# Optimization experiments

Measured on AMD Instinct MI355X. Metric: run time of the kernel, lower is better.

Reference implementation:

```python
import jax, jax.numpy as jnp
import numpy as np

N_EMBD = 2048
N_HEAD = 16
HEAD_SIZE = N_EMBD // N_HEAD


def setup_inputs() -> dict:
    key = jax.random.key(0)
    k1, k2, k3 = jax.random.split(key, 3)
    x = jax.random.normal(k1, (4, 2048, N_EMBD), dtype=jnp.float32)
    # Linear weights stored as (in, out) for x @ W
    scale = 1.0 / np.sqrt(N_EMBD)
    w_qkv = jax.random.normal(k2, (N_EMBD, 3 * N_EMBD), dtype=jnp.float32) * scale
    w_proj = jax.random.normal(k3, (N_EMBD, N_EMBD), dtype=jnp.float32) * scale
    return {"x": x, "w_qkv": w_qkv, "w_proj": w_proj}


def reference(x, w_qkv, w_proj):
    B, T, C = x.shape
    qkv = x @ w_qkv  # [B, T, 3C]
    q, k, v = jnp.split(qkv, 3, axis=-1)
    # [B, H, T, Dh]
    def heads(t):
        return t.reshape(B, T, N_HEAD, HEAD_SIZE).transpose(0, 2, 1, 3)
    q, k, v = heads(q), heads(k), heads(v)
    scores = jnp.einsum('bhqd,bhkd->bhqk', q, k) * (1.0 / np.sqrt(HEAD_SIZE))
    causal = jnp.tril(jnp.ones((T, T), dtype=bool))
    scores = jnp.where(causal, scores, jnp.finfo(scores.dtype).min)
    att = jax.nn.softmax(scores, axis=-1)
    y = jnp.einsum('bhqk,bhkd->bhqd', att, v)
    y = y.transpose(0, 2, 1, 3).reshape(B, T, C)
    return y @ w_proj
```

## Files before the change

### kernel.cpp

```cpp
#include <hip/hip_runtime.h>

typedef unsigned short u16;
typedef unsigned int u32;
typedef __bf16 bf16x8 __attribute__((ext_vector_type(8)));
typedef float f32x4 __attribute__((ext_vector_type(4)));
typedef u32 u32x4 __attribute__((ext_vector_type(4)));

__device__ __forceinline__ u16 f2bf(float f) {
  u32 u = __builtin_bit_cast(u32, f);
  return (u16)((u + 0x7fffu + ((u >> 16) & 1u)) >> 16);
}

__device__ __forceinline__ f32x4 mfma16(bf16x8 a, bf16x8 b, f32x4 c) {
  return __builtin_amdgcn_mfma_f32_16x16x32_bf16(a, b, c, 0, 0, 0);
}

__device__ __forceinline__ u32 cvtpk_bf16(float lo, float hi) {
  u32 r;
  asm("v_cvt_pk_bf16_f32 %0, %1, %2" : "=v"(r) : "v"(lo), "v"(hi));
  return r;
}

__device__ __forceinline__ float fexp2(float x) {
  float r;
  asm("v_exp_f32 %0, %1" : "=v"(r) : "v"(x));
  return r;
}

struct alignas(8) U16x4 { u16 x, y, z, w; };

#define AS1 __attribute__((address_space(1)))
#define AS3 __attribute__((address_space(3)))
__device__ __forceinline__ void gl16(const u16* g, u16* l) {
  __builtin_amdgcn_global_load_lds((const AS1 u32*)g, (AS3 u32*)l, 16, 0, 0);
}

__global__ __launch_bounds__(256) void k_f32_to_bf16(const float* __restrict__ in,
                                                     u16* __restrict__ out, long n4) {
  long i = (long)blockIdx.x * blockDim.x + threadIdx.x;
  long stride = (long)gridDim.x * blockDim.x;
  for (; i < n4; i += stride) {
    float4 v = ((const float4*)in)[i];
    U16x4 o{f2bf(v.x), f2bf(v.y), f2bf(v.z), f2bf(v.w)};
    ((U16x4*)out)[i] = o;
  }
}

__global__ __launch_bounds__(256) void k_transpose_f32_to_bf16(const float* __restrict__ in,
                                                               u16* __restrict__ out,
                                                               int rows, int cols) {
  __shared__ float tile[64][65];
  int bc = blockIdx.x * 64, br = blockIdx.y * 64;
  int tx = threadIdx.x & 15;
  int ty = threadIdx.x >> 4;
#pragma unroll
  for (int i = 0; i < 4; ++i) {
    int r = ty + i * 16;
    float4 v = *(const float4*)&in[(long)(br + r) * cols + bc + tx * 4];
    tile[r][tx * 4 + 0] = v.x;
    tile[r][tx * 4 + 1] = v.y;
    tile[r][tx * 4 + 2] = v.z;
    tile[r][tx * 4 + 3] = v.w;
  }
  __syncthreads();
#pragma unroll
  for (int i = 0; i < 4; ++i) {
    int c = ty + i * 16;
    int r4 = tx * 4;
    U16x4 o{f2bf(tile[r4 + 0][c]), f2bf(tile[r4 + 1][c]),
            f2bf(tile[r4 + 2][c]), f2bf(tile[r4 + 3][c])};
    *(U16x4*)&out[(long)(bc + c) * rows + br + r4] = o;
  }
}

template <typename OutT, bool WRITE_VT>
__global__ __launch_bounds__(512, 2) void k_gemm256(const u16* __restrict__ A,
                                                    const u16* __restrict__ Bt,
                                                    OutT* __restrict__ C,
                                                    u16* __restrict__ vt,
                                                    int M, int N, int K) {
  __shared__ alignas(16) u16 As[4][8192];
  __shared__ alignas(16) u16 Bs[4][8192];

  int gx = gridDim.x;
  int nwg = gx * gridDim.y;
  int bid = blockIdx.y * gx + blockIdx.x;
  int swz = (bid & 7) * (nwg >> 3) + (bid >> 3);
  int rem = swz % (gx * 4);
  int bx = rem >> 2;
  int by = (swz / (gx * 4)) * 4 + (rem & 3);

  int tid = threadIdx.x;
  int lane = tid & 63;
  int w = tid >> 6;
  int wr = w >> 2, wc = w & 3;
  int lr = lane & 15, lg = lane >> 4;
  long brow = (long)by * 256, bcol = (long)bx * 256;

  int rS[2], cS[2];
#pragma unroll
  for (int i = 0; i < 2; ++i) {
    int q = i * 512 + tid;
    rS[i] = q >> 2;
    cS[i] = ((q & 3) ^ ((rS[i] >> 1) & 3)) << 3;
  }
  const u16* Ab = A + brow * K;
  const u16* Bb = Bt + bcol * K;

  int offA[8], offB[4];
#pragma unroll
  for (int m = 0; m < 8; ++m) {
    int row = wr * 128 + m * 16 + lr;
    offA[m] = row * 32 + ((lg ^ ((row >> 1) & 3)) << 3);
  }
#pragma unroll
  for (int n = 0; n < 4; ++n) {
    int row = wc * 64 + n * 16 + lr;
    offB[n] = row * 32 + ((lg ^ ((row >> 1) & 3)) << 3);
  }

  f32x4 zero = {0.f, 0.f, 0.f, 0.f};
  f32x4 acc[8][4];
#pragma unroll
  for (int m = 0; m < 8; ++m)
#pragma unroll
    for (int n = 0; n < 4; ++n) acc[m][n] = zero;

  int NS = K >> 5;

#define STAGE256(SBUF, KT)                                                          \
  do {                                                                              \
    int kk_ = (KT) << 5;                                                            \
    gl16(Ab + (long)rS[0] * K + kk_ + cS[0], &As[SBUF][(0 * 512 + w * 64) * 8]);    \
    gl16(Ab + (long)rS[1] * K + kk_ + cS[1], &As[SBUF][(1 * 512 + w * 64) * 8]);    \
    gl16(Bb + (long)rS[0] * K + kk_ + cS[0], &Bs[SBUF][(0 * 512 + w * 64) * 8]);    \
    gl16(Bb + (long)rS[1] * K + kk_ + cS[1], &Bs[SBUF][(1 * 512 + w * 64) * 8]);    \
  } while (0)

  STAGE256(0, 0);
  STAGE256(1, 1);
  STAGE256(2, 2);
  asm volatile("s_waitcnt vmcnt(8)" ::: "memory");
  __builtin_amdgcn_s_barrier();

  for (int s = 0; s < NS; ++s) {
    int cb = s & 3;
    bf16x8 af[8], bfn[4];
#pragma unroll
    for (int m = 0; m < 8; ++m) af[m] = *(const bf16x8*)&As[cb][offA[m]];
#pragma unroll
    for (int n = 0; n < 4; ++n) bfn[n] = *(const bf16x8*)&Bs[cb][offB[n]];
    int t = s + 3;
    int tb = t & 3;
    if (t > NS - 1) t = NS - 1;
    STAGE256(tb, t);
    __builtin_amdgcn_s_setprio(1);
#pragma unroll
    for (int m = 0; m < 4; ++m)
#pragma unroll
      for (int n = 0; n < 4; ++n) acc[m][n] = mfma16(af[m], bfn[n], acc[m][n]);
    __builtin_amdgcn_s_setprio(0);
    __builtin_amdgcn_s_setprio(1);
#pragma unroll
    for (int m = 4; m < 8; ++m)
#pragma unroll
      for (int n = 0; n < 4; ++n) acc[m][n] = mfma16(af[m], bfn[n], acc[m][n]);
    __builtin_amdgcn_s_setprio(0);
    asm volatile("s_waitcnt vmcnt(8)" ::: "memory");
    __builtin_amdgcn_s_barrier();
  }
#undef STAGE256
  asm volatile("s_waitcnt vmcnt(0)" ::: "memory");

  if constexpr (WRITE_VT) {
    if (bcol >= 4096) {
      int b_ = (int)(brow >> 11);
      int tb_ = (int)(brow & 2047) + wr * 128;
#pragma unroll
      for (int m = 0; m < 8; ++m)
#pragma unroll
        for (int n = 0; n < 4; ++n) {
          int hd = (int)(bcol - 4096) + wc * 64 + n * 16 + lr;
          int h_ = hd >> 7, d_ = hd & 127;
          U16x4 pk{f2bf(acc[m][n][0]), f2bf(acc[m][n][1]),
                   f2bf(acc[m][n][2]), f2bf(acc[m][n][3])};
          *(U16x4*)(vt + ((long)(b_ * 16 + h_) * 128 + d_) * 2048 + tb_ + m * 16 + lg * 4) = pk;
        }
      return;
    }
  }
#pragma unroll
  for (int m = 0; m < 8; ++m)
#pragma unroll
    for (int n = 0; n < 4; ++n)
#pragma unroll
      for (int r = 0; r < 4; ++r) {
        long row = brow + wr * 128 + m * 16 + lg * 4 + r;
        long col = bcol + wc * 64 + n * 16 + lr;
        float v = acc[m][n][r];
        if constexpr (sizeof(OutT) == 2)
          C[row * N + col] = (OutT)f2bf(v);
        else
          C[row * N + col] = v;
      }
}

__global__ __launch_bounds__(256, 2) void k_attn2(const u16* __restrict__ qkv,
                                                  const u16* __restrict__ vt,
                                                  u16* __restrict__ y) {
  __shared__ alignas(16) u16 Ks[2][64 * 128];
  __shared__ alignas(16) u16 Vs[2][128 * 64];

  int bh = blockIdx.x;
  int qb = 15 - (int)blockIdx.y;
  int b = bh >> 4, h = bh & 15;
  int tid = threadIdx.x;
  int lane = tid & 63;
  int w = tid >> 6;
  int lr = lane & 15, lg = lane >> 4;
  int x7 = lr & 7;
  bool hiA = (lane & 32) != 0;
  bool hiB = (lane & 16) != 0;
  const float scale2 = 0.08838834764831845f * 1.4426950408889634f;

  const u16* kbase = qkv + (long)(b * 2048) * 6144 + 2048 + h * 128;
  const u16* vtbh = vt + (long)bh * 128 * 2048;
  int qbase = qb * 128 + w * 32;

  const u16* qptr = qkv + (long)(qb * 128 + b * 2048) * 6144 + h * 128;
  bf16x8 qf[2][4];
  for (int qsub = 0; qsub < 2; ++qsub)
    for (int dc = 0; dc < 4; ++dc)
      qf[qsub][dc] = *(const bf16x8*)(qptr + (long)(w * 32 + qsub * 16 + lr) * 6144 + dc * 32 + lg * 8);

  f32x4 zero = {0.f, 0.f, 0.f, 0.f};
  f32x4 o[2][8];
  for (int qs = 0; qs < 2; ++qs)
    for (int ds = 0; ds < 8; ++ds) o[qs][ds] = zero;
  float m_run[2] = {-1e30f, -1e30f};
  float l_run[2] = {0.f, 0.f};

  int nkt = 2 * qb + 2;
  int qmaxw = qbase + 31;

#define STAGE_K(BUF, KT)                                                        \
  do {                                                                          \
    for (int i_ = 0; i_ < 4; ++i_) {                                            \
      int rl_ = w * 16 + i_ * 4;                                                \
      int row_ = rl_ + (lane >> 4);                                             \
      int ch_ = (lane & 15) ^ (row_ & 7);                                       \
      gl16(kbase + (long)((KT)*64 + row_) * 6144 + ch_ * 8, &Ks[BUF][rl_ * 128]); \
    }                                                                           \
  } while (0)

#define STAGE_V(BUF, KT)                                                        \
  do {                                                                          \
    for (int i_ = 0; i_ < 4; ++i_) {                                            \
      int dl_ = w * 32 + i_ * 8;                                                \
      int d_ = dl_ + (lane >> 3);                                               \
      int ch_ = (lane & 7) ^ (d_ & 7);                                          \
      gl16(vtbh + (long)d_ * 2048 + (KT)*64 + ch_ * 8, &Vs[BUF][dl_ * 64]);     \
    }                                                                           \
  } while (0)

#define QKPART(BUF, KT, PA, MASKED)                                             \
  do {                                                                          \
    const u16* Kb = &Ks[BUF][0];                                                \
    f32x4 s[2][4];                                                              \
    for (int qs = 0; qs < 2; ++qs)                                              \
      for (int ks = 0; ks < 4; ++ks) s[qs][ks] = zero;                          \
    for (int ks = 0; ks < 4; ++ks) {                                            \
      int row = ks * 16 + lr;                                                   \
      for (int dc = 0; dc < 4; ++dc) {                                          \
        bf16x8 kf = *(const bf16x8*)(Kb + row * 128 + ((dc * 4 + lg) ^ x7) * 8); \
        s[0][ks] = mfma16(kf, qf[0][dc], s[0][ks]);                             \
        s[1][ks] = mfma16(kf, qf[1][dc], s[1][ks]);                             \
      }                                                                         \
    }                                                                           \
    for (int qs = 0; qs < 2; ++qs) {                                            \
      int qg = qbase + qs * 16 + lr;                                            \
      float p[16];                                                              \
      float tmax = -1e30f;                                                      \
      for (int ks = 0; ks < 4; ++ks)                                            \
        for (int r = 0; r < 4; ++r) {                                           \
          float v = s[qs][ks][r] * scale2;                                      \
          if (MASKED) {                                                         \
            int key = (KT)*64 + ks * 16 + lg * 4 + r;                           \
            v = (key <= qg) ? v : -1e30f;                                       \
          }                                                                     \
          p[ks * 4 + r] = v;                                                    \
          tmax = fmaxf(tmax, v);                                                \
        }                                                                       \
      tmax = fmaxf(tmax, __shfl_xor(tmax, 16));                                 \
      tmax = fmaxf(tmax, __shfl_xor(tmax, 32));                                 \
      float m_new = fmaxf(m_run[qs], tmax);                                     \
      float alpha = fexp2(m_run[qs] - m_new);                                   \
      float psum = 0.f;                                                         \
      for (int i = 0; i < 16; ++i) {                                            \
        p[i] = fexp2(p[i] - m_new);                                             \
        psum += p[i];                                                           \
      }                                                                         \
      psum += __shfl_xor(psum, 16);                                             \
      psum += __shfl_xor(psum, 32);                                             \
      l_run[qs] = l_run[qs] * alpha + psum;                                     \
      m_run[qs] = m_new;                                                        \
       \
       \
      for (int j = 0; j < 2; ++j) {                                             \
        u32 w0 = cvtpk_bf16(p[j * 8 + 0], p[j * 8 + 1]);                        \
        u32 w1 = cvtpk_bf16(p[j * 8 + 2], p[j * 8 + 3]);                        \
        u32 w2 = cvtpk_bf16(p[j * 8 + 4], p[j * 8 + 5]);                        \
        u32 w3 = cvtpk_bf16(p[j * 8 + 6], p[j * 8 + 7]);                        \
        u32 a0 = hiA ? w0 : w2, a1 = hiA ? w1 : w3;                             \
        u32 r0 = __shfl_xor(a0, 32), r1 = __shfl_xor(a1, 32);                   \
        u32 q0 = hiA ? r0 : w0, q1 = hiA ? r1 : w1;                             \
        u32 q2 = hiA ? w2 : r0, q3 = hiA ? w3 : r1;                             \
        u32 s0 = hiB ? q0 : q2, s1 = hiB ? q1 : q3;                             \
        u32 t0 = __shfl_xor(s0, 16), t1 = __shfl_xor(s1, 16);                   \
        u32x4 fw;                                                               \
        fw[0] = hiB ? t0 : q0;                                                  \
        fw[1] = hiB ? t1 : q1;                                                  \
        fw[2] = hiB ? q2 : t0;                                                  \
        fw[3] = hiB ? q3 : t1;                                                  \
        PA[qs][j] = __builtin_bit_cast(bf16x8, fw);                             \
      }                                                                         \
      float alr[4];                                                             \
      for (int r = 0; r < 4; ++r) alr[r] = __shfl(alpha, lg * 4 + r);           \
      for (int ds = 0; ds < 8; ++ds)                                            \
        for (int r = 0; r < 4; ++r) o[qs][ds][r] *= alr[r];                     \
    }                                                                           \
  } while (0)

#define PVPART(BUF, PA)                                                         \
  do {                                                                          \
    const u16* Vb = &Vs[BUF][0];                                                \
    for (int j = 0; j < 2; ++j) {                                               \
      int chv = ((j * 4 + lg) ^ x7) * 8;                                        \
      for (int ds = 0; ds < 8; ++ds) {                                          \
        bf16x8 vf = *(const bf16x8*)(Vb + (ds * 16 + lr) * 64 + chv);           \
        o[0][ds] = mfma16(PA[0][j], vf, o[0][ds]);                              \
        o[1][ds] = mfma16(PA[1][j], vf, o[1][ds]);                              \
      }                                                                         \
    }                                                                           \
  } while (0)

  STAGE_K(0, 0);
  STAGE_V(0, 0);
  asm volatile("s_waitcnt vmcnt(4)" ::: "memory");
  __builtin_amdgcn_s_barrier();

  for (int t = 0; t < nkt; ++t) {
    int tn = (t + 1 < nkt) ? t + 1 : nkt - 1;
    int nb = (t + 1) & 1;
    bool live = (t * 64 <= qmaxw);
    bool masked = (t >= 2 * qb);
    bf16x8 pa[2][2];
    STAGE_K(nb, tn);
    if (live) {
      if (masked) QKPART(t & 1, t, pa, 1);
      else        QKPART(t & 1, t, pa, 0);
    }
    STAGE_V(nb, tn);
    asm volatile("s_waitcnt vmcnt(8)" ::: "memory");
    __builtin_amdgcn_s_barrier();
    if (live) PVPART(t & 1, pa);
    asm volatile("s_waitcnt vmcnt(4)" ::: "memory");
    __builtin_amdgcn_s_barrier();
  }
  asm volatile("s_waitcnt vmcnt(0)" ::: "memory");
#undef STAGE_K
#undef STAGE_V
#undef QKPART
#undef PVPART

  float linv[2][4];
  for (int qs = 0; qs < 2; ++qs)
    for (int r = 0; r < 4; ++r) linv[qs][r] = 1.0f / __shfl(l_run[qs], lg * 4 + r);
  u16* yb = y + (long)(b * 2048 + qb * 128 + w * 32) * 2048 + h * 128;
  for (int qs = 0; qs < 2; ++qs)
    for (int ds = 0; ds < 8; ++ds)
      for (int r = 0; r < 4; ++r)
        yb[(long)(qs * 16 + lg * 4 + r) * 2048 + ds * 16 + lr] = f2bf(o[qs][ds][r] * linv[qs][r]);
}

extern "C" void kernel_launch(void* const* d_in, const int* in_sizes, int n_in,
                              void* d_out, int out_size, void* d_ws, size_t ws_size,
                              hipStream_t stream) {
  const float* x = (const float*)d_in[0];
  const float* w_qkv = (const float*)d_in[1];
  const float* w_proj = (const float*)d_in[2];
  float* out = (float*)d_out;

  char* ws = (char*)d_ws;
  if (ws_size < 201326592ull) return;
  u16* QKV = (u16*)(ws);
  u16* WqT = (u16*)(ws + 100663296);
  u16* WpT = (u16*)(ws + 125829120);
  u16* Xb  = (u16*)(ws + 134217728);
  u16* Vt  = (u16*)(ws + 167772160);

  k_f32_to_bf16<<<2048, 256, 0, stream>>>(x, Xb, (8192L * 2048) / 4);
  k_transpose_f32_to_bf16<<<dim3(96, 32), 256, 0, stream>>>(w_qkv, WqT, 2048, 6144);
  k_transpose_f32_to_bf16<<<dim3(32, 32), 256, 0, stream>>>(w_proj, WpT, 2048, 2048);

  k_gemm256<u16, true><<<dim3(24, 32), 512, 0, stream>>>(Xb, WqT, QKV, Vt, 8192, 6144, 2048);

  k_attn2<<<dim3(64, 16), 256, 0, stream>>>(QKV, Vt, Xb );

  k_gemm256<float, false><<<dim3(8, 32), 512, 0, stream>>>(Xb, WpT, out, nullptr, 8192, 2048, 2048);
}
```

Baseline: 394.1 us.

## Merge prep kernels into one launch and skip softmax rescale when max unchanged

The three preprocessing kernels (x conversion and two weight transposes) are merged into a single k_prep launch, with block ranges picking the task, to save two kernel launches and their tail gaps. In the attention softmax, a wave-wide vote checks whether the running max grew. If it did not, the alpha exp, the alpha shuffles and the rescale of the output accumulators are skipped. This adds a wave vote and a branch per tile, and the prep blocks now share one launch shape.

```diff
diff --git a/kernel.cpp b/kernel.cpp
--- a/kernel.cpp
+++ b/kernel.cpp
@@ -35,24 +35,14 @@
   __builtin_amdgcn_global_load_lds((const AS1 u32*)g, (AS3 u32*)l, 16, 0, 0);
 }
 
-__global__ __launch_bounds__(256) void k_f32_to_bf16(const float* __restrict__ in,
-                                                     u16* __restrict__ out, long n4) {
-  long i = (long)blockIdx.x * blockDim.x + threadIdx.x;
-  long stride = (long)gridDim.x * blockDim.x;
-  for (; i < n4; i += stride) {
-    float4 v = ((const float4*)in)[i];
-    U16x4 o{f2bf(v.x), f2bf(v.y), f2bf(v.z), f2bf(v.w)};
-    ((U16x4*)out)[i] = o;
-  }
-}
-
-__global__ __launch_bounds__(256) void k_transpose_f32_to_bf16(const float* __restrict__ in,
-                                                               u16* __restrict__ out,
-                                                               int rows, int cols) {
+__device__ __forceinline__ void transpose_tile(const float* __restrict__ in,
+                                               u16* __restrict__ out,
+                                               int rows, int cols, int bx, int by,
+                                               int tidx) {
   __shared__ float tile[64][65];
-  int bc = blockIdx.x * 64, br = blockIdx.y * 64;
-  int tx = threadIdx.x & 15;
-  int ty = threadIdx.x >> 4;
+  int bc = bx * 64, br = by * 64;
+  int tx = tidx & 15;
+  int ty = tidx >> 4;
 #pragma unroll
   for (int i = 0; i < 4; ++i) {
     int r = ty + i * 16;
@@ -70,6 +60,32 @@
     U16x4 o{f2bf(tile[r4 + 0][c]), f2bf(tile[r4 + 1][c]),
             f2bf(tile[r4 + 2][c]), f2bf(tile[r4 + 3][c])};
     *(U16x4*)&out[(long)(bc + c) * rows + br + r4] = o;
+  }
+}
+
+__global__ __launch_bounds__(256) void k_prep(const float* __restrict__ x,
+                                              u16* __restrict__ xb,
+                                              const float* __restrict__ wqkv,
+                                              u16* __restrict__ wqt,
+                                              const float* __restrict__ wproj,
+                                              u16* __restrict__ wpt) {
+  int bid = blockIdx.x;
+  int tid = threadIdx.x;
+  if (bid < 2048) {
+    long n4 = (8192L * 2048) / 4;
+    long i = (long)bid * 256 + tid;
+    long stride = 2048L * 256;
+    for (; i < n4; i += stride) {
+      float4 v = ((const float4*)x)[i];
+      U16x4 o{f2bf(v.x), f2bf(v.y), f2bf(v.z), f2bf(v.w)};
+      ((U16x4*)xb)[i] = o;
+    }
+  } else if (bid < 5120) {
+    int idx = bid - 2048;
+    transpose_tile(wqkv, wqt, 2048, 6144, idx % 96, idx / 96, tid);
+  } else {
+    int idx = bid - 5120;
+    transpose_tile(wproj, wpt, 2048, 2048, idx % 32, idx / 32, tid);
   }
 }
 
@@ -293,8 +309,9 @@
         }                                                                       \
       tmax = fmaxf(tmax, __shfl_xor(tmax, 16));                                 \
       tmax = fmaxf(tmax, __shfl_xor(tmax, 32));                                 \
-      float m_new = fmaxf(m_run[qs], tmax);                                     \
-      float alpha = fexp2(m_run[qs] - m_new);                                   \
+        \
+      bool noresc = (__all(tmax <= m_run[qs]) != 0);                            \
+      float m_new = noresc ? m_run[qs] : fmaxf(m_run[qs], tmax);                \
       float psum = 0.f;                                                         \
       for (int i = 0; i < 16; ++i) {                                            \
         p[i] = fexp2(p[i] - m_new);                                             \
@@ -302,8 +319,17 @@
       }                                                                         \
       psum += __shfl_xor(psum, 16);                                             \
       psum += __shfl_xor(psum, 32);                                             \
-      l_run[qs] = l_run[qs] * alpha + psum;                                     \
-      m_run[qs] = m_new;                                                        \
+      if (noresc) {                                                             \
+        l_run[qs] = l_run[qs] + psum;                                           \
+      } else {                                                                  \
+        float alpha = fexp2(m_run[qs] - m_new);                                 \
+        l_run[qs] = l_run[qs] * alpha + psum;                                   \
+        m_run[qs] = m_new;                                                      \
+        float alr[4];                                                           \
+        for (int r = 0; r < 4; ++r) alr[r] = __shfl(alpha, lg * 4 + r);         \
+        for (int ds = 0; ds < 8; ++ds)                                          \
+          for (int r = 0; r < 4; ++r) o[qs][ds][r] *= alr[r];                   \
+      }                                                                         \
        \
        \
       for (int j = 0; j < 2; ++j) {                                             \
@@ -324,10 +350,6 @@
         fw[3] = hiB ? q3 : t1;                                                  \
         PA[qs][j] = __builtin_bit_cast(bf16x8, fw);                             \
       }                                                                         \
-      float alr[4];                                                             \
-      for (int r = 0; r < 4; ++r) alr[r] = __shfl(alpha, lg * 4 + r);           \
-      for (int ds = 0; ds < 8; ++ds)                                            \
-        for (int r = 0; r < 4; ++r) o[qs][ds][r] *= alr[r];                     \
     }                                                                           \
   } while (0)
 
@@ -399,9 +421,7 @@
   u16* Xb  = (u16*)(ws + 134217728);
   u16* Vt  = (u16*)(ws + 167772160);
 
-  k_f32_to_bf16<<<2048, 256, 0, stream>>>(x, Xb, (8192L * 2048) / 4);
-  k_transpose_f32_to_bf16<<<dim3(96, 32), 256, 0, stream>>>(w_qkv, WqT, 2048, 6144);
-  k_transpose_f32_to_bf16<<<dim3(32, 32), 256, 0, stream>>>(w_proj, WpT, 2048, 2048);
+  k_prep<<<6144, 256, 0, stream>>>(x, Xb, w_qkv, WqT, w_proj, WpT);
 
   k_gemm256<u16, true><<<dim3(24, 32), 512, 0, stream>>>(Xb, WqT, QKV, Vt, 8192, 6144, 2048);
 
```

New measurement: 395.7 us, median of 2. About the same (+0.4%).
